# Kernel optimization log

Hardware: AMD Instinct MI355X
Metric: run time of the kernel (lower is better)

The kernel has to match this reference:

```python
import jax, jax.numpy as jnp
import numpy as np

HID = 256
FC1_OUT = 256


def setup_inputs() -> dict:
    key = jax.random.key(0)
    k1, k2, k3, k4, k5 = jax.random.split(key, 5)
    B, S = 64, 4096
    trg = jax.random.normal(k1, (B, S, HID), dtype=jnp.float32)
    src = jax.random.normal(k2, (B, 128, HID), dtype=jnp.float32)
    # fc_1: Linear(hid_dim, 256); fc_2: Linear(256, 1). PyTorch default init ~ U(-1/sqrt(fan_in), 1/sqrt(fan_in)).
    s1 = 1.0 / np.sqrt(HID)
    s2 = 1.0 / np.sqrt(FC1_OUT)
    W1 = jax.random.uniform(k3, (HID, FC1_OUT), minval=-s1, maxval=s1, dtype=jnp.float32)
    b1 = jnp.zeros((FC1_OUT,), dtype=jnp.float32)
    W2 = jax.random.uniform(k4, (FC1_OUT, 1), minval=-s2, maxval=s2, dtype=jnp.float32)
    b2 = jnp.zeros((1,), dtype=jnp.float32)
    return {"trg": trg, "src": src, "W1": W1, "b1": b1, "W2": W2, "b2": b2}


def reference(trg, src, W1, b1, W2, b2):
    # n_layers = 0: decoder layers are identity; src is unused.
    # Norm-weighted softmax pooling over the atom (sequence) dimension.
    norm = jnp.linalg.norm(trg, axis=2)            # [B, S]
    w = jax.nn.softmax(norm, axis=1)               # [B, S]
    pooled = jnp.einsum('bs,bsh->bh', w, trg)      # [B, hid] — replaces the double Python loop
    h = jax.nn.relu(pooled @ W1 + b1)              # dropout = identity at inference
    label = h @ W2 + b2                            # [B, 1]
    return label
```

## Files before the change

kernel.cpp:

```cpp
#include <hip/hip_runtime.h>
#include <math.h>

#define BATCH 64
#define SEQ   4096
#define HID   256
#define NBLK  32
#define ROWS_PER_BLK (SEQ / NBLK)
#define THREADS 256
#define NWAVE (THREADS / 64)
#define GSZ   8
#define NGRP  (THREADS / GSZ)
#define ITERS (ROWS_PER_BLK / NGRP)
#define VPL   (HID / (GSZ * 4))

__global__ __launch_bounds__(THREADS) void pool_pass(
        const float* __restrict__ trg,
        float* __restrict__ ws_m,
        float* __restrict__ ws_l,
        float* __restrict__ ws_p) {
    const int b     = blockIdx.x / NBLK;
    const int chunk = blockIdx.x % NBLK;
    const int tid   = threadIdx.x;
    const int gid   = tid >> 3;
    const int sub   = tid & 7;

    const float* base = trg + ((size_t)b * SEQ + (size_t)chunk * ROWS_PER_BLK) * HID;

    float m = -INFINITY, l = 0.f;
    float4 acc[VPL];
    #pragma unroll
    for (int q = 0; q < VPL; ++q) acc[q] = make_float4(0.f, 0.f, 0.f, 0.f);

    #pragma unroll 1
    for (int t = 0; t < ITERS; ++t) {
        const float* rp = base + (size_t)(t * NGRP + gid) * HID + sub * 4;
        float4 v[VPL];
        #pragma unroll
        for (int q = 0; q < VPL; ++q)
            v[q] = *reinterpret_cast<const float4*>(rp + q * (GSZ * 4));

        float ss = 0.f;
        #pragma unroll
        for (int q = 0; q < VPL; ++q)
            ss += v[q].x * v[q].x + v[q].y * v[q].y
                + v[q].z * v[q].z + v[q].w * v[q].w;
        ss += __shfl_xor(ss, 1, 64);
        ss += __shfl_xor(ss, 2, 64);
        ss += __shfl_xor(ss, 4, 64);
        const float nrm = sqrtf(ss);

        if (nrm > m + 8.f) {
            const float sc = __expf(m - nrm);
            l *= sc;
            #pragma unroll
            for (int q = 0; q < VPL; ++q) {
                acc[q].x *= sc; acc[q].y *= sc;
                acc[q].z *= sc; acc[q].w *= sc;
            }
            m = nrm;
        }
        const float p = __expf(nrm - m);
        l += p;
        #pragma unroll
        for (int q = 0; q < VPL; ++q) {
            acc[q].x = fmaf(p, v[q].x, acc[q].x);
            acc[q].y = fmaf(p, v[q].y, acc[q].y);
            acc[q].z = fmaf(p, v[q].z, acc[q].z);
            acc[q].w = fmaf(p, v[q].w, acc[q].w);
        }
    }

    __shared__ float s_m[NGRP];
    __shared__ float s_l[NGRP];
    __shared__ float s_p[NGRP][HID];
    if (sub == 0) s_m[gid] = m;
    __syncthreads();
    float m_blk = s_m[0];
    #pragma unroll
    for (int g = 1; g < NGRP; ++g) m_blk = fmaxf(m_blk, s_m[g]);
    const float sc = __expf(m - m_blk);
    if (sub == 0) s_l[gid] = l * sc;
    #pragma unroll
    for (int q = 0; q < VPL; ++q) {
        float4 a = acc[q];
        a.x *= sc; a.y *= sc; a.z *= sc; a.w *= sc;
        *reinterpret_cast<float4*>(&s_p[gid][q * (GSZ * 4) + sub * 4]) = a;
    }
    __syncthreads();

    const int j = tid;
    float pj = 0.f;
    #pragma unroll
    for (int g = 0; g < NGRP; ++g) pj += s_p[g][j];
    const int pidx = b * NBLK + chunk;
    ws_p[(size_t)pidx * HID + j] = pj;
    if (j == 0) {
        ws_m[pidx] = m_blk;
        float lt = 0.f;
        #pragma unroll
        for (int g = 0; g < NGRP; ++g) lt += s_l[g];
        ws_l[pidx] = lt;
    }
}

__global__ __launch_bounds__(THREADS) void finish_pass(
        const float* __restrict__ ws_m,
        const float* __restrict__ ws_l,
        const float* __restrict__ ws_p,
        const float* __restrict__ W1,
        const float* __restrict__ b1,
        const float* __restrict__ W2,
        const float* __restrict__ b2,
        float* __restrict__ out) {
    const int b = blockIdx.x;
    const int j = threadIdx.x;

    __shared__ float s_m[NBLK];
    __shared__ float s_l[NBLK];
    __shared__ float s_pooled[HID];
    __shared__ float s_red[NWAVE];

    if (j < NBLK) {
        s_m[j] = ws_m[b * NBLK + j];
        s_l[j] = ws_l[b * NBLK + j];
    }
    __syncthreads();

    float m = s_m[0];
    #pragma unroll
    for (int i = 1; i < NBLK; ++i) m = fmaxf(m, s_m[i]);

    float l = 0.f, pj = 0.f;
    #pragma unroll 8
    for (int i = 0; i < NBLK; ++i) {
        const float sc = __expf(s_m[i] - m);
        l  += s_l[i] * sc;
        pj += ws_p[(size_t)(b * NBLK + i) * HID + j] * sc;
    }
    const float pooled = pj / l;
    s_pooled[j] = pooled;
    __syncthreads();

    float h = b1[j];
    #pragma unroll 8
    for (int k = 0; k < HID; ++k)
        h = fmaf(s_pooled[k], W1[k * HID + j], h);
    h = fmaxf(h, 0.f);

    float v = h * W2[j];
    #pragma unroll
    for (int off = 32; off > 0; off >>= 1)
        v += __shfl_xor(v, off, 64);
    if ((j & 63) == 0) s_red[j >> 6] = v;
    __syncthreads();
    if (j == 0)
        out[b] = s_red[0] + s_red[1] + s_red[2] + s_red[3] + b2[0];
}

extern "C" void kernel_launch(void* const* d_in, const int* in_sizes, int n_in,
                              void* d_out, int out_size, void* d_ws, size_t ws_size,
                              hipStream_t stream) {
    const float* trg = (const float*)d_in[0];
    const float* W1  = (const float*)d_in[2];
    const float* b1  = (const float*)d_in[3];
    const float* W2  = (const float*)d_in[4];
    const float* b2  = (const float*)d_in[5];
    float* out = (float*)d_out;

    float* ws_m = (float*)d_ws;
    float* ws_l = ws_m + BATCH * NBLK;
    float* ws_p = ws_l + BATCH * NBLK;

    pool_pass<<<dim3(BATCH * NBLK), THREADS, 0, stream>>>(trg, ws_m, ws_l, ws_p);
    finish_pass<<<dim3(BATCH), THREADS, 0, stream>>>(ws_m, ws_l, ws_p,
                                                     W1, b1, W2, b2, out);
}
```

Measured before the change: 58.07 us.

## Reduce pool partials with wave shuffles and precompute softmax scales in finish

The per-block epilogue of pool_pass now merges the 8 row groups in each wave with cross-lane shuffles instead of writing all 32 group partials to shared memory. Only 4 per-wave partials go to LDS, which shrinks shared memory and the 32-way reduction loop, and the occupancy hint in launch_bounds is raised. In finish_pass the per-chunk exp scales are computed once into shared memory and the W1 loop unroll is increased. The cost is many extra shuffles in the epilogue, while the main streaming loop, which dominates, is unchanged.

```diff
diff --git a/kernel.cpp b/kernel.cpp
--- a/kernel.cpp
+++ b/kernel.cpp
@@ -13,7 +13,7 @@
 #define ITERS (ROWS_PER_BLK / NGRP)
 #define VPL   (HID / (GSZ * 4))
 
-__global__ __launch_bounds__(THREADS) void pool_pass(
+__global__ __launch_bounds__(THREADS, 8) void pool_pass(
         const float* __restrict__ trg,
         float* __restrict__ ws_m,
         float* __restrict__ ws_l,
@@ -21,8 +21,11 @@
     const int b     = blockIdx.x / NBLK;
     const int chunk = blockIdx.x % NBLK;
     const int tid   = threadIdx.x;
+    const int wave  = tid >> 6;
+    const int lane  = tid & 63;
     const int gid   = tid >> 3;
     const int sub   = tid & 7;
+    const int gw    = gid & 7;
 
     const float* base = trg + ((size_t)b * SEQ + (size_t)chunk * ROWS_PER_BLK) * HID;
 
@@ -70,36 +73,58 @@
         }
     }
 
-    __shared__ float s_m[NGRP];
-    __shared__ float s_l[NGRP];
-    __shared__ float s_p[NGRP][HID];
-    if (sub == 0) s_m[gid] = m;
-    __syncthreads();
-    float m_blk = s_m[0];
-    #pragma unroll
-    for (int g = 1; g < NGRP; ++g) m_blk = fmaxf(m_blk, s_m[g]);
-    const float sc = __expf(m - m_blk);
-    if (sub == 0) s_l[gid] = l * sc;
+    float m_w = m;
+    m_w = fmaxf(m_w, __shfl_xor(m_w, 8, 64));
+    m_w = fmaxf(m_w, __shfl_xor(m_w, 16, 64));
+    m_w = fmaxf(m_w, __shfl_xor(m_w, 32, 64));
+    const float sc = __expf(m - m_w);
+    float l_w = l * sc;
+    l_w += __shfl_xor(l_w, 8, 64);
+    l_w += __shfl_xor(l_w, 16, 64);
+    l_w += __shfl_xor(l_w, 32, 64);
     #pragma unroll
     for (int q = 0; q < VPL; ++q) {
         float4 a = acc[q];
         a.x *= sc; a.y *= sc; a.z *= sc; a.w *= sc;
-        *reinterpret_cast<float4*>(&s_p[gid][q * (GSZ * 4) + sub * 4]) = a;
-    }
+        a.x += __shfl_xor(a.x, 8, 64);
+        a.y += __shfl_xor(a.y, 8, 64);
+        a.z += __shfl_xor(a.z, 8, 64);
+        a.w += __shfl_xor(a.w, 8, 64);
+        a.x += __shfl_xor(a.x, 16, 64);
+        a.y += __shfl_xor(a.y, 16, 64);
+        a.z += __shfl_xor(a.z, 16, 64);
+        a.w += __shfl_xor(a.w, 16, 64);
+        a.x += __shfl_xor(a.x, 32, 64);
+        a.y += __shfl_xor(a.y, 32, 64);
+        a.z += __shfl_xor(a.z, 32, 64);
+        a.w += __shfl_xor(a.w, 32, 64);
+        acc[q] = a;
+    }
+
+    float4 mine = acc[0];
+    #pragma unroll
+    for (int q = 1; q < VPL; ++q) if (gw == q) mine = acc[q];
+
+    __shared__ float s_p[NWAVE][HID];
+    __shared__ float s_m[NWAVE];
+    __shared__ float s_l[NWAVE];
+    *reinterpret_cast<float4*>(&s_p[wave][gw * 32 + sub * 4]) = mine;
+    if (lane == 0) { s_m[wave] = m_w; s_l[wave] = l_w; }
     __syncthreads();
 
     const int j = tid;
-    float pj = 0.f;
-    #pragma unroll
-    for (int g = 0; g < NGRP; ++g) pj += s_p[g][j];
+    const float m_blk = fmaxf(fmaxf(s_m[0], s_m[1]), fmaxf(s_m[2], s_m[3]));
+    const float e0 = __expf(s_m[0] - m_blk);
+    const float e1 = __expf(s_m[1] - m_blk);
+    const float e2 = __expf(s_m[2] - m_blk);
+    const float e3 = __expf(s_m[3] - m_blk);
+    const float pj = e0 * s_p[0][j] + e1 * s_p[1][j]
+                   + e2 * s_p[2][j] + e3 * s_p[3][j];
     const int pidx = b * NBLK + chunk;
     ws_p[(size_t)pidx * HID + j] = pj;
     if (j == 0) {
         ws_m[pidx] = m_blk;
-        float lt = 0.f;
-        #pragma unroll
-        for (int g = 0; g < NGRP; ++g) lt += s_l[g];
-        ws_l[pidx] = lt;
+        ws_l[pidx] = e0 * s_l[0] + e1 * s_l[1] + e2 * s_l[2] + e3 * s_l[3];
     }
 }
 
@@ -117,6 +142,7 @@
 
     __shared__ float s_m[NBLK];
     __shared__ float s_l[NBLK];
+    __shared__ float s_scale[NBLK];
     __shared__ float s_pooled[HID];
     __shared__ float s_red[NWAVE];
 
@@ -129,20 +155,20 @@
     float m = s_m[0];
     #pragma unroll
     for (int i = 1; i < NBLK; ++i) m = fmaxf(m, s_m[i]);
+    if (j < NBLK) s_scale[j] = __expf(s_m[j] - m);
+    __syncthreads();
 
     float l = 0.f, pj = 0.f;
     #pragma unroll 8
     for (int i = 0; i < NBLK; ++i) {
-        const float sc = __expf(s_m[i] - m);
-        l  += s_l[i] * sc;
-        pj += ws_p[(size_t)(b * NBLK + i) * HID + j] * sc;
-    }
-    const float pooled = pj / l;
-    s_pooled[j] = pooled;
+        l  = fmaf(s_l[i], s_scale[i], l);
+        pj = fmaf(ws_p[(size_t)(b * NBLK + i) * HID + j], s_scale[i], pj);
+    }
+    s_pooled[j] = pj / l;
     __syncthreads();
 
     float h = b1[j];
-    #pragma unroll 8
+    #pragma unroll 16
     for (int k = 0; k < HID; ++k)
         h = fmaf(s_pooled[k], W1[k * HID + j], h);
     h = fmaxf(h, 0.f);
```

New measurement: 170.9 us. 194% more time.
